# Optimization experiments

Measured on AMD Instinct MI355X. Metric: run time of the kernel, lower is better.

## Reference

```python
import jax, jax.numpy as jnp
import numpy as np

N_BITS = 8  # abits = wbits = 8 (symmetric signed per-tensor quant)
QN = -2 ** (N_BITS - 1)
QP = 2 ** (N_BITS - 1) - 1


def _round_pass(v):
    # straight-through round: forward round, backward identity
    return v + jax.lax.stop_gradient(jnp.round(v) - v)


def _quantize(t):
    # per-tensor symmetric quantization; scale detached like torch .detach()
    scale = jax.lax.stop_gradient(jnp.max(jnp.abs(t))) / QP
    q = _round_pass(jnp.clip(t / scale, QN, QP))
    return q, scale


def _quantized_linear(x3, s_x, w, b):
    # x3: [B, S, Din]; w: [Dout, Din]; b: [Dout]; s_x: scalar dequant scale
    B, S, Din = x3.shape
    x2 = x3.reshape(-1, Din) * s_x              # dequantize incoming activations
    qw, sw = _quantize(w)
    qx, sx = _quantize(x2)
    out = jnp.matmul(qx, qw.T)                  # int-valued float GEMM
    out = out + b[None, :]                      # bias added before rescale (as in source)
    return (out * (sw * sx)).reshape(B, S, -1)


def setup_inputs() -> dict:
    key = jax.random.key(0)
    k1, k2, k3, k4, k5 = jax.random.split(key, 5)
    B, S, D, H = 128, 197, 384, 1536
    x = jax.random.normal(k1, (B, S, D), dtype=jnp.float32)
    act_scaling_factor = jnp.ones((1,), dtype=jnp.float32)
    w1 = jax.random.normal(k2, (H, D), dtype=jnp.float32) * (1.0 / np.sqrt(D))
    b1 = jax.random.normal(k3, (H,), dtype=jnp.float32) * 0.02
    w2 = jax.random.normal(k4, (D, H), dtype=jnp.float32) * (1.0 / np.sqrt(H))
    b2 = jax.random.normal(k5, (D,), dtype=jnp.float32) * 0.02
    return {"x": x, "act_scaling_factor": act_scaling_factor,
            "w1": w1, "b1": b1, "w2": w2, "b2": b2}


def reference(x, act_scaling_factor, w1, b1, w2, b2):
    s_x = act_scaling_factor.reshape(())
    h = _quantized_linear(x, s_x, w1, b1)       # fc1
    h = jax.nn.gelu(h, approximate=False)       # torch nn.GELU (erf)
    qh, s_h = _quantize(h)                      # qact1: requantize activations
    out = _quantized_linear(qh, s_h, w2, b2)    # fc2
    return out
```

## Files before the change

### kernel.cpp

```cpp
#include <hip/hip_runtime.h>
#include <hip/hip_bf16.h>
#include <stdint.h>

typedef int v4i __attribute__((ext_vector_type(4)));

#define GPTR(p) ((const __attribute__((address_space(1))) void*)(p))
#define LPTR(p) ((__attribute__((address_space(3))) void*)(p))

__device__ __forceinline__ float wave_max(float m) {
#pragma unroll
  for (int off = 32; off > 0; off >>= 1)
    m = fmaxf(m, __shfl_xor(m, off, 64));
  return m;
}

__device__ __forceinline__ float fast_erf(float x) {
  const float ax = fabsf(x);
  const float t = __builtin_amdgcn_rcpf(fmaf(0.3275911f, ax, 1.0f));
  float p = fmaf(1.061405429f, t, -1.453152027f);
  p = fmaf(p, t, 1.421413741f);
  p = fmaf(p, t, -0.284496736f);
  p = fmaf(p, t, 0.254829592f);
  const float e = __expf(-ax * ax);
  const float r = 1.0f - p * t * e;
  return copysignf(r, x);
}

__device__ __forceinline__ float gelu_exact(float f) {
  return 0.5f * f * (1.0f + fast_erf(f * 0.70710678118654752f));
}

__global__ void absmax3_kernel(const float* __restrict__ x, int nx4,
                               const float* __restrict__ smul,
                               const float* __restrict__ w1, int nw14,
                               const float* __restrict__ w2, int nw24,
                               unsigned* __restrict__ scal) {
  __shared__ float red[4];
  const int bid = blockIdx.x;
  const float4* s4;
  int n4, b0, nb;
  float s = 1.0f;
  unsigned* dst;
  if (bid < 512)      { s4 = (const float4*)x;  n4 = nx4;  s = smul[0]; dst = scal;     b0 = bid;       nb = 512; }
  else if (bid < 640) { s4 = (const float4*)w1; n4 = nw14;              dst = scal + 1; b0 = bid - 512; nb = 128; }
  else                { s4 = (const float4*)w2; n4 = nw24;              dst = scal + 2; b0 = bid - 640; nb = 128; }
  float m = 0.0f;
  const int stride = nb * blockDim.x;
  for (int i = b0 * blockDim.x + threadIdx.x; i < n4; i += stride) {
    float4 v = s4[i];
    m = fmaxf(m, fabsf(v.x * s));
    m = fmaxf(m, fabsf(v.y * s));
    m = fmaxf(m, fabsf(v.z * s));
    m = fmaxf(m, fabsf(v.w * s));
  }
  m = wave_max(m);
  if ((threadIdx.x & 63) == 0) red[threadIdx.x >> 6] = m;
  __syncthreads();
  if (threadIdx.x == 0)
    atomicMax(dst, __float_as_uint(fmaxf(fmaxf(red[0], red[1]), fmaxf(red[2], red[3]))));
}

__global__ void quantize3_kernel(const float* __restrict__ x, int nx4,
                                 const float* __restrict__ smul,
                                 const float* __restrict__ w1, int nw14,
                                 const float* __restrict__ w2, int nw24,
                                 const unsigned* __restrict__ scal,
                                 int8_t* __restrict__ qx,
                                 int8_t* __restrict__ qw1,
                                 int8_t* __restrict__ qw2) {
  const int bid = blockIdx.x;
  const float4* s4;
  char4* d4;
  int n4, b0, nb;
  float s = 1.0f, mx;
  if (bid < 2048)      { s4 = (const float4*)x;  d4 = (char4*)qx;  n4 = nx4;  s = smul[0]; mx = __uint_as_float(scal[0]); b0 = bid;        nb = 2048; }
  else if (bid < 2176) { s4 = (const float4*)w1; d4 = (char4*)qw1; n4 = nw14;              mx = __uint_as_float(scal[1]); b0 = bid - 2048; nb = 128; }
  else                 { s4 = (const float4*)w2; d4 = (char4*)qw2; n4 = nw24;              mx = __uint_as_float(scal[2]); b0 = bid - 2176; nb = 128; }
  const float scale = mx / 127.0f;
  const int stride = nb * blockDim.x;
  for (int i = b0 * blockDim.x + threadIdx.x; i < n4; i += stride) {
    float4 v = s4[i];
    char4 qq;
    qq.x = (signed char)(int)rintf(fminf(fmaxf((v.x * s) / scale, -128.0f), 127.0f));
    qq.y = (signed char)(int)rintf(fminf(fmaxf((v.y * s) / scale, -128.0f), 127.0f));
    qq.z = (signed char)(int)rintf(fminf(fmaxf((v.z * s) / scale, -128.0f), 127.0f));
    qq.w = (signed char)(int)rintf(fminf(fmaxf((v.w * s) / scale, -128.0f), 127.0f));
    d4[i] = qq;
  }
}

__global__ void reduce_scale_kernel(const float* __restrict__ partial, int n,
                                    unsigned* __restrict__ scal) {
  __shared__ float red[4];
  float m = -3.4e38f;
  for (int i = threadIdx.x; i < n; i += blockDim.x) m = fmaxf(m, partial[i]);
  m = wave_max(m);
  if ((threadIdx.x & 63) == 0) red[threadIdx.x >> 6] = m;
  __syncthreads();
  if (threadIdx.x == 0) {
    m = fmaxf(fmaxf(red[0], red[1]), fmaxf(red[2], red[3]));
    const float sx = __uint_as_float(scal[0]) / 127.0f;
    const float sw = __uint_as_float(scal[1]) / 127.0f;
    const float max_f = m * (sw * sx);
    scal[3] = __float_as_uint(fmaxf(gelu_exact(max_f), 0.1699702f));
  }
}

template <int EPI>
__global__ __launch_bounds__(256, 4)
void gemm_i8_kernel(const int8_t* __restrict__ A, const int8_t* __restrict__ B,
                    const float* __restrict__ bias,
                    const unsigned* __restrict__ scal,
                    float* __restrict__ partial,
                    int8_t* __restrict__ out_i8,
                    float* __restrict__ out_f32,
                    int N, int K, int GN) {
  __shared__ __align__(16) int8_t lA[2][128 * 64];
  __shared__ __align__(16) int8_t lB[2][128 * 64];
  __shared__ float red[4];

  const int nwg = gridDim.x;
  const int q = nwg >> 3, rr = nwg & 7;
  const int xcd = blockIdx.x & 7, sub = blockIdx.x >> 3;
  const int wg = (xcd < rr ? xcd * (q + 1) : rr * (q + 1) + (xcd - rr) * q) + sub;
  const int bx = wg % GN;
  const int by = wg / GN;

  const int t = threadIdx.x;
  const int lane = t & 63;
  const int wave = t >> 6;
  const int wr = wave >> 1;
  const int wc = wave & 1;
  const size_t m0 = (size_t)by * 128;
  const int n0 = bx * 128;

  const int8_t* Ab = A + m0 * (size_t)K;
  const int8_t* Bb = B + (size_t)n0 * (size_t)K;

  v4i acc[4][4] = {};
  const int KT = K >> 6;

  const int row0 = t >> 2;
  const int ss = (t & 3) ^ ((row0 >> 1) & 3);
  const int ubase = __builtin_amdgcn_readfirstlane((t & 192) * 16);
  const size_t srcA0 = (size_t)row0 * K + (size_t)(ss * 16);
  const size_t srcA1 = (size_t)(row0 + 64) * K + (size_t)(ss * 16);

  auto stage = [&](int buf, int kt) {
    const int8_t* ga = Ab + kt * 64;
    const int8_t* gb = Bb + kt * 64;
    __builtin_amdgcn_global_load_lds(GPTR(ga + srcA0), LPTR(&lA[buf][ubase]), 16, 0, 0);
    __builtin_amdgcn_global_load_lds(GPTR(ga + srcA1), LPTR(&lA[buf][4096 + ubase]), 16, 0, 0);
    __builtin_amdgcn_global_load_lds(GPTR(gb + srcA0), LPTR(&lB[buf][ubase]), 16, 0, 0);
    __builtin_amdgcn_global_load_lds(GPTR(gb + srcA1), LPTR(&lB[buf][4096 + ubase]), 16, 0, 0);
  };

  const int r15 = lane & 15;
  const int q4 = lane >> 4;

  auto compute = [&](int buf) {
    v4i af[4], bf[4];
#pragma unroll
    for (int fr = 0; fr < 4; ++fr) {
      const int row = wr * 64 + fr * 16 + r15;
      const int slot = q4 ^ ((row >> 1) & 3);
      af[fr] = *(const v4i*)(&lA[buf][row * 64 + slot * 16]);
    }
#pragma unroll
    for (int fc = 0; fc < 4; ++fc) {
      const int row = wc * 64 + fc * 16 + r15;
      const int slot = q4 ^ ((row >> 1) & 3);
      bf[fc] = *(const v4i*)(&lB[buf][row * 64 + slot * 16]);
    }
#pragma unroll
    for (int fr = 0; fr < 4; ++fr)
#pragma unroll
      for (int fc = 0; fc < 4; ++fc)
        acc[fr][fc] = __builtin_amdgcn_mfma_i32_16x16x64_i8(af[fr], bf[fc], acc[fr][fc], 0, 0, 0);
  };

  stage(0, 0);
  asm volatile("s_waitcnt vmcnt(0)" ::: "memory");
  __syncthreads();
  int cur = 0;
  for (int kt = 1; kt < KT; ++kt) {
    stage(cur ^ 1, kt);
    compute(cur);
    __syncthreads();
    cur ^= 1;
  }
  compute(cur);

  const int rb = q4 * 4;

  if constexpr (EPI == 0) {
    float lm = -3.4e38f;
#pragma unroll
    for (int fc = 0; fc < 4; ++fc) {
      int im = acc[0][fc][0];
#pragma unroll
      for (int fr = 0; fr < 4; ++fr)
#pragma unroll
        for (int r = 0; r < 4; ++r) im = max(im, acc[fr][fc][r]);
      const float bv = bias[n0 + wc * 64 + fc * 16 + r15];
      lm = fmaxf(lm, (float)im + bv);
    }
    lm = wave_max(lm);
    if (lane == 0) red[wave] = lm;
    __syncthreads();
    if (t == 0)
      partial[wg] = fmaxf(fmaxf(red[0], red[1]), fmaxf(red[2], red[3]));
  } else if constexpr (EPI == 1) {
    const float sx = __uint_as_float(scal[0]) / 127.0f;
    const float sw = __uint_as_float(scal[1]) / 127.0f;
    const float s1 = sw * sx;
    const float sh = __uint_as_float(scal[3]) / 127.0f;
    const float inv_sh = __builtin_amdgcn_rcpf(sh);
#pragma unroll
    for (int fc = 0; fc < 4; ++fc) {
      const int n = n0 + wc * 64 + fc * 16 + r15;
      const float bv = bias[n];
#pragma unroll
      for (int fr = 0; fr < 4; ++fr) {
#pragma unroll
        for (int r = 0; r < 4; ++r) {
          const size_t m = m0 + (size_t)(wr * 64 + fr * 16 + rb + r);
          const float f = ((float)acc[fr][fc][r] + bv) * s1;
          const float g = gelu_exact(f);
          const float qv = rintf(fminf(fmaxf(g * inv_sh, -128.0f), 127.0f));
          out_i8[m * (size_t)N + n] = (int8_t)(int)qv;
        }
      }
    }
  } else {
    const float sw2 = __uint_as_float(scal[2]) / 127.0f;
    const float sh = __uint_as_float(scal[3]) / 127.0f;
    const float x2max = 127.0f * sh;
    const float sx2 = x2max / 127.0f;
    const float s2 = sw2 * sx2;
#pragma unroll
    for (int fc = 0; fc < 4; ++fc) {
      const int n = n0 + wc * 64 + fc * 16 + r15;
      const float bv = bias[n];
#pragma unroll
      for (int fr = 0; fr < 4; ++fr) {
#pragma unroll
        for (int r = 0; r < 4; ++r) {
          const size_t m = m0 + (size_t)(wr * 64 + fr * 16 + rb + r);
          out_f32[m * (size_t)N + n] = ((float)acc[fr][fc][r] + bv) * s2;
        }
      }
    }
  }
}

extern "C" void kernel_launch(void* const* d_in, const int* in_sizes, int n_in,
                              void* d_out, int out_size, void* d_ws, size_t ws_size,
                              hipStream_t stream) {
  const float* x   = (const float*)d_in[0];
  const float* sxp = (const float*)d_in[1];
  const float* w1  = (const float*)d_in[2];
  const float* b1  = (const float*)d_in[3];
  const float* w2  = (const float*)d_in[4];
  const float* b2  = (const float*)d_in[5];

  const int H = in_sizes[3];
  const int D = in_sizes[5];
  const int M = in_sizes[0] / D;
  const int GM = M / 128;
  const int GN1 = H / 128;
  const int GN2 = D / 128;

  uint8_t* ws = (uint8_t*)d_ws;
  unsigned* scal = (unsigned*)ws;
  size_t off = 256;
  float* partial = (float*)(ws + off); off += 16384;
  int8_t* qx  = (int8_t*)(ws + off); off += (size_t)M * D;
  int8_t* qw1 = (int8_t*)(ws + off); off += (size_t)H * D;
  int8_t* qw2 = (int8_t*)(ws + off); off += (size_t)D * H;
  int8_t* qh  = (int8_t*)(ws + off); off += (size_t)M * H;
  (void)ws_size; (void)n_in; (void)out_size;

  hipMemsetAsync(scal, 0, 16, stream);

  absmax3_kernel<<<dim3(768), dim3(256), 0, stream>>>(
      x, M * D / 4, sxp, w1, H * D / 4, w2, D * H / 4, scal);

  quantize3_kernel<<<dim3(2304), dim3(256), 0, stream>>>(
      x, M * D / 4, sxp, w1, H * D / 4, w2, D * H / 4, scal, qx, qw1, qw2);

  dim3 blk(256);
  dim3 g1(GN1 * GM);
  gemm_i8_kernel<0><<<g1, blk, 0, stream>>>(qx, qw1, b1, scal, partial, nullptr, nullptr, H, D, GN1);
  reduce_scale_kernel<<<1, 256, 0, stream>>>(partial, GM * GN1, scal);
  gemm_i8_kernel<1><<<g1, blk, 0, stream>>>(qx, qw1, b1, scal, nullptr, qh, nullptr, H, D, GN1);

  dim3 g2(GN2 * GM);
  gemm_i8_kernel<2><<<g2, blk, 0, stream>>>(qh, qw2, b2, scal, nullptr, nullptr, (float*)d_out, D, H, GN2);
}
```

Before: 131.7 us.

## Use 64-row tiles for fc2 GEMM and stage fc1 int8 output through LDS

New measurement: 137.6 us. +4.5%, slower.

```diff
diff --git a/kernel.cpp b/kernel.cpp
--- a/kernel.cpp
+++ b/kernel.cpp
@@ -106,8 +106,8 @@
   }
 }
 
-template <int EPI>
-__global__ __launch_bounds__(256, 4)
+template <int EPI, int BM>
+__global__ __launch_bounds__(256, BM == 128 ? 4 : 5)
 void gemm_i8_kernel(const int8_t* __restrict__ A, const int8_t* __restrict__ B,
                     const float* __restrict__ bias,
                     const unsigned* __restrict__ scal,
@@ -115,9 +115,10 @@
                     int8_t* __restrict__ out_i8,
                     float* __restrict__ out_f32,
                     int N, int K, int GN) {
-  __shared__ __align__(16) int8_t lA[2][128 * 64];
+  constexpr int FR = BM / 32;
+  constexpr int AH = BM / 64;
+  __shared__ __align__(16) int8_t lA[2][BM * 64];
   __shared__ __align__(16) int8_t lB[2][128 * 64];
-  __shared__ float red[4];
 
   const int nwg = gridDim.x;
   const int q = nwg >> 3, rr = nwg & 7;
@@ -131,13 +132,13 @@
   const int wave = t >> 6;
   const int wr = wave >> 1;
   const int wc = wave & 1;
-  const size_t m0 = (size_t)by * 128;
+  const size_t m0 = (size_t)by * BM;
   const int n0 = bx * 128;
 
   const int8_t* Ab = A + m0 * (size_t)K;
   const int8_t* Bb = B + (size_t)n0 * (size_t)K;
 
-  v4i acc[4][4] = {};
+  v4i acc[FR][4] = {};
   const int KT = K >> 6;
 
   const int row0 = t >> 2;
@@ -150,7 +151,8 @@
     const int8_t* ga = Ab + kt * 64;
     const int8_t* gb = Bb + kt * 64;
     __builtin_amdgcn_global_load_lds(GPTR(ga + srcA0), LPTR(&lA[buf][ubase]), 16, 0, 0);
-    __builtin_amdgcn_global_load_lds(GPTR(ga + srcA1), LPTR(&lA[buf][4096 + ubase]), 16, 0, 0);
+    if constexpr (AH == 2)
+      __builtin_amdgcn_global_load_lds(GPTR(ga + srcA1), LPTR(&lA[buf][4096 + ubase]), 16, 0, 0);
     __builtin_amdgcn_global_load_lds(GPTR(gb + srcA0), LPTR(&lB[buf][ubase]), 16, 0, 0);
     __builtin_amdgcn_global_load_lds(GPTR(gb + srcA1), LPTR(&lB[buf][4096 + ubase]), 16, 0, 0);
   };
@@ -159,10 +161,10 @@
   const int q4 = lane >> 4;
 
   auto compute = [&](int buf) {
-    v4i af[4], bf[4];
-#pragma unroll
-    for (int fr = 0; fr < 4; ++fr) {
-      const int row = wr * 64 + fr * 16 + r15;
+    v4i af[FR], bf[4];
+#pragma unroll
+    for (int fr = 0; fr < FR; ++fr) {
+      const int row = wr * (BM / 2) + fr * 16 + r15;
       const int slot = q4 ^ ((row >> 1) & 3);
       af[fr] = *(const v4i*)(&lA[buf][row * 64 + slot * 16]);
     }
@@ -173,7 +175,7 @@
       bf[fc] = *(const v4i*)(&lB[buf][row * 64 + slot * 16]);
     }
 #pragma unroll
-    for (int fr = 0; fr < 4; ++fr)
+    for (int fr = 0; fr < FR; ++fr)
 #pragma unroll
       for (int fc = 0; fc < 4; ++fc)
         acc[fr][fc] = __builtin_amdgcn_mfma_i32_16x16x64_i8(af[fr], bf[fc], acc[fr][fc], 0, 0, 0);
@@ -199,13 +201,15 @@
     for (int fc = 0; fc < 4; ++fc) {
       int im = acc[0][fc][0];
 #pragma unroll
-      for (int fr = 0; fr < 4; ++fr)
+      for (int fr = 0; fr < FR; ++fr)
 #pragma unroll
         for (int r = 0; r < 4; ++r) im = max(im, acc[fr][fc][r]);
       const float bv = bias[n0 + wc * 64 + fc * 16 + r15];
       lm = fmaxf(lm, (float)im + bv);
     }
     lm = wave_max(lm);
+    __syncthreads();
+    float* red = (float*)lA;
     if (lane == 0) red[wave] = lm;
     __syncthreads();
     if (t == 0)
@@ -216,21 +220,33 @@
     const float s1 = sw * sx;
     const float sh = __uint_as_float(scal[3]) / 127.0f;
     const float inv_sh = __builtin_amdgcn_rcpf(sh);
+    __syncthreads();
+    int8_t* qt = (int8_t*)lA;
 #pragma unroll
     for (int fc = 0; fc < 4; ++fc) {
-      const int n = n0 + wc * 64 + fc * 16 + r15;
-      const float bv = bias[n];
+      const int col = wc * 64 + fc * 16 + r15;
+      const float bv = bias[n0 + col];
+      const float bvs = bv * s1;
 #pragma unroll
       for (int fr = 0; fr < 4; ++fr) {
+        const int rowb = wr * 64 + fr * 16 + rb;
 #pragma unroll
         for (int r = 0; r < 4; ++r) {
-          const size_t m = m0 + (size_t)(wr * 64 + fr * 16 + rb + r);
-          const float f = ((float)acc[fr][fc][r] + bv) * s1;
+          const float f = fmaf((float)acc[fr][fc][r], s1, bvs);
           const float g = gelu_exact(f);
           const float qv = rintf(fminf(fmaxf(g * inv_sh, -128.0f), 127.0f));
-          out_i8[m * (size_t)N + n] = (int8_t)(int)qv;
+          qt[(rowb + r) * 128 + (col ^ (q4 << 4))] = (int8_t)(int)qv;
         }
       }
+    }
+    __syncthreads();
+#pragma unroll
+    for (int v = 0; v < 4; ++v) {
+      const int row = v * 32 + (t >> 3);
+      const int colb = (t & 7) * 16;
+      const int swz = ((row >> 2) & 3) << 4;
+      *(v4i*)(out_i8 + (m0 + row) * (size_t)N + n0 + colb) =
+          *(const v4i*)(qt + row * 128 + (colb ^ swz));
     }
   } else {
     const float sw2 = __uint_as_float(scal[2]) / 127.0f;
@@ -242,12 +258,13 @@
     for (int fc = 0; fc < 4; ++fc) {
       const int n = n0 + wc * 64 + fc * 16 + r15;
       const float bv = bias[n];
-#pragma unroll
-      for (int fr = 0; fr < 4; ++fr) {
+      const float bvs = bv * s2;
+#pragma unroll
+      for (int fr = 0; fr < FR; ++fr) {
 #pragma unroll
         for (int r = 0; r < 4; ++r) {
-          const size_t m = m0 + (size_t)(wr * 64 + fr * 16 + rb + r);
-          out_f32[m * (size_t)N + n] = ((float)acc[fr][fc][r] + bv) * s2;
+          const size_t m = m0 + (size_t)(wr * (BM / 2) + fr * 16 + rb + r);
+          out_f32[m * (size_t)N + n] = fmaf((float)acc[fr][fc][r], s2, bvs);
         }
       }
     }
@@ -267,7 +284,8 @@
   const int H = in_sizes[3];
   const int D = in_sizes[5];
   const int M = in_sizes[0] / D;
-  const int GM = M / 128;
+  const int GM1 = M / 128;
+  const int GM2 = M / 64;
   const int GN1 = H / 128;
   const int GN2 = D / 128;
 
@@ -290,11 +308,11 @@
       x, M * D / 4, sxp, w1, H * D / 4, w2, D * H / 4, scal, qx, qw1, qw2);
 
   dim3 blk(256);
-  dim3 g1(GN1 * GM);
-  gemm_i8_kernel<0><<<g1, blk, 0, stream>>>(qx, qw1, b1, scal, partial, nullptr, nullptr, H, D, GN1);
-  reduce_scale_kernel<<<1, 256, 0, stream>>>(partial, GM * GN1, scal);
-  gemm_i8_kernel<1><<<g1, blk, 0, stream>>>(qx, qw1, b1, scal, nullptr, qh, nullptr, H, D, GN1);
-
-  dim3 g2(GN2 * GM);
-  gemm_i8_kernel<2><<<g2, blk, 0, stream>>>(qh, qw2, b2, scal, nullptr, nullptr, (float*)d_out, D, H, GN2);
-}
+  dim3 g1(GN1 * GM1);
+  gemm_i8_kernel<0, 128><<<g1, blk, 0, stream>>>(qx, qw1, b1, scal, partial, nullptr, nullptr, H, D, GN1);
+  reduce_scale_kernel<<<1, 256, 0, stream>>>(partial, GM1 * GN1, scal);
+  gemm_i8_kernel<1, 128><<<g1, blk, 0, stream>>>(qx, qw1, b1, scal, nullptr, qh, nullptr, H, D, GN1);
+
+  dim3 g2(GN2 * GM2);
+  gemm_i8_kernel<2, 64><<<g2, blk, 0, stream>>>(qh, qw2, b2, scal, nullptr, nullptr, (float*)d_out, D, H, GN2);
+}
```
